# Kernel optimization log

Hardware: AMD Instinct MI355X
Metric: run time of the kernel (lower is better)

The kernel has to match this reference:

```python
import jax, jax.numpy as jnp
import numpy as np

N, E, D, H = 8192, 8, 2048, 2048


def setup_inputs() -> dict:
    key = jax.random.key(0)
    k1, k2, k3, k4 = jax.random.split(key, 4)
    x = jax.random.normal(k1, (N, D), dtype=jnp.float32)
    indices = jax.random.randint(k2, (N, 1), 0, E)  # top_k=1 expert assignment
    W = jax.random.normal(k3, (E, D, H), dtype=jnp.float32) * 0.02
    b = jax.random.normal(k4, (E, H), dtype=jnp.float32) * 0.02
    return {"x": x, "indices": indices, "W": W, "b": b}


def reference(x, indices, W, b):
    # Each token is routed to exactly one expert (top_k=1):
    # expert_id[n] = indices[n, 0]. The torch module loops experts e=0..E-1,
    # gathers tokens with (indices == e).any(-1) (ascending order via nonzero),
    # applies expert e's Linear + ReLU, and concatenates outputs in expert order.
    expert_id = indices[:, 0]                              # [N]
    # Dense dispatch: compute every expert's linear on every token, then pick
    # each token's own expert row (jit-friendly; no data-dependent shapes).
    y_all = jnp.einsum('nd,edh->neh', x, W) + b[None, :, :]  # [N, E, H]
    y = jnp.take_along_axis(y_all, expert_id[:, None, None], axis=1)[:, 1 - 1, :]  # [N, H]
    y = jax.nn.relu(y)
    # Concat in expert order == stable sort of tokens by expert id
    # (nonzero returns ascending indices, so within-expert order is preserved).
    order = jnp.argsort(expert_id)  # stable by default
    return y[order]
```

## Files before the change

### kernel.cpp

```cpp
#include <hip/hip_runtime.h>

#define N_TOK 8192
#define N_EXP 8
#define DIM   2048
#define HID   2048

typedef __attribute__((ext_vector_type(8))) short short8;
typedef __attribute__((ext_vector_type(4))) float f32x4;
typedef __attribute__((ext_vector_type(4))) unsigned short ushort4v;

__device__ inline unsigned short f2bf(float f) {
  unsigned int u = __builtin_bit_cast(unsigned int, f);
  unsigned int r = u + 0x7FFFu + ((u >> 16) & 1u);
  return (unsigned short)(r >> 16);
}

__global__ __launch_bounds__(256) void sort_experts(const int* __restrict__ idx,
                                                    int* __restrict__ perm,
                                                    int* __restrict__ offs) {
  __shared__ int cnt[256][8];
  __shared__ int base[8];
  const int t = threadIdx.x;
  int local[8] = {0,0,0,0,0,0,0,0};
  const int r0 = t * 32;
  for (int i = 0; i < 32; ++i) {
    int e = idx[r0 + i] & 7;
    ++local[e];
  }
#pragma unroll
  for (int e = 0; e < 8; ++e) cnt[t][e] = local[e];
  __syncthreads();
  if (t < 8) {
    int s = 0;
    for (int i = 0; i < 256; ++i) { int v = cnt[i][t]; cnt[i][t] = s; s += v; }
    base[t] = s;
  }
  __syncthreads();
  if (t == 0) {
    int s = 0;
    for (int e = 0; e < 8; ++e) { int v = base[e]; offs[e] = s; base[e] = s; s += v; }
    offs[8] = s;
  }
  __syncthreads();
  int pos[8];
#pragma unroll
  for (int e = 0; e < 8; ++e) pos[e] = base[e] + cnt[t][e];
  for (int i = 0; i < 32; ++i) {
    int r = r0 + i;
    int e = idx[r] & 7;
    perm[pos[e]++] = r;
  }
}

__global__ __launch_bounds__(256) void gather_convert_x(const float* __restrict__ x,
                                                        const int* __restrict__ perm,
                                                        unsigned short* __restrict__ xs) {
  int gid = blockIdx.x * 256 + threadIdx.x;
  int p = gid >> 8;
  int c = gid & 255;
  int src = perm[p];
  const float* sp = x + (size_t)src * DIM + c * 8;
  float4 a = *(const float4*)sp;
  float4 b = *(const float4*)(sp + 4);
  short8 o;
  o[0] = (short)f2bf(a.x); o[1] = (short)f2bf(a.y);
  o[2] = (short)f2bf(a.z); o[3] = (short)f2bf(a.w);
  o[4] = (short)f2bf(b.x); o[5] = (short)f2bf(b.y);
  o[6] = (short)f2bf(b.z); o[7] = (short)f2bf(b.w);
  *(short8*)(xs + (size_t)p * DIM + c * 8) = o;
}

__global__ __launch_bounds__(256) void transpose_convert_w(const float* __restrict__ W,
                                                           unsigned short* __restrict__ Wt) {
  __shared__ unsigned short tile[64][68];
  const int e = blockIdx.z;
  const int d0 = blockIdx.y * 64;
  const int h0 = blockIdx.x * 64;
  const int t = threadIdx.x;
  const int cr = t & 15;
  const int rr = t >> 4;
  const float* Wp = W + ((size_t)e * DIM + d0) * HID + h0;
#pragma unroll
  for (int i = 0; i < 4; ++i) {
    int d = rr + i * 16;
    float4 v = *(const float4*)(Wp + (size_t)d * HID + cr * 4);
    ushort4v o;
    o[0] = f2bf(v.x); o[1] = f2bf(v.y); o[2] = f2bf(v.z); o[3] = f2bf(v.w);
    *(ushort4v*)&tile[d][cr * 4] = o;
  }
  __syncthreads();
  unsigned short* op = Wt + ((size_t)e * HID + h0) * DIM + d0;
#pragma unroll
  for (int i = 0; i < 4; ++i) {
    int h = rr + i * 16;
    ushort4v o;
    o[0] = tile[cr * 4 + 0][h];
    o[1] = tile[cr * 4 + 1][h];
    o[2] = tile[cr * 4 + 2][h];
    o[3] = tile[cr * 4 + 3][h];
    *(ushort4v*)(op + (size_t)h * DIM + cr * 4) = o;
  }
}

#define BM 128
#define BN 128
#define BK 32

__global__ __launch_bounds__(256) void grouped_gemm(const unsigned short* __restrict__ xs,
                                                    const unsigned short* __restrict__ Wt,
                                                    const float* __restrict__ bias,
                                                    const int* __restrict__ offs,
                                                    float* __restrict__ out) {
  const int e   = blockIdx.z;
  const int off = offs[e];
  const int cnt = offs[e + 1] - off;
  const int mt  = blockIdx.y;
  if (mt * BM >= cnt) return;
  const int n0 = blockIdx.x * BN;

  __shared__ __align__(16) unsigned short As[BM * BK];
  __shared__ __align__(16) unsigned short Bs[BN * BK];

  const int t    = threadIdx.x;
  const int wid  = t >> 6;
  const int lane = t & 63;
  const int wr   = wid >> 1, wc = wid & 1;
  const int l15  = lane & 15;
  const int l4   = lane >> 4;

  f32x4 acc[4][4] = {};

  size_t srcA[2], srcB[2];
  const size_t WtE = (size_t)e * DIM * HID;
#pragma unroll
  for (int c = 0; c < 2; ++c) {
    int lin = c * 256 + t;
    int r = lin >> 2, kq = lin & 3;
    int p = off + mt * BM + r;
    if (p > N_TOK - 1) p = N_TOK - 1;
    srcA[c] = (size_t)p * DIM + kq * 8;
    srcB[c] = WtE + (size_t)(n0 + r) * DIM + kq * 8;
  }

  for (int k0 = 0; k0 < DIM; k0 += BK) {
#pragma unroll
    for (int c = 0; c < 2; ++c) {
      __builtin_amdgcn_global_load_lds(
          (const __attribute__((address_space(1))) void*)(xs + srcA[c] + k0),
          (__attribute__((address_space(3))) void*)(As + c * 2048 + t * 8), 16, 0, 0);
      __builtin_amdgcn_global_load_lds(
          (const __attribute__((address_space(1))) void*)(Wt + srcB[c] + k0),
          (__attribute__((address_space(3))) void*)(Bs + c * 2048 + t * 8), 16, 0, 0);
    }
    __syncthreads();

    short8 af[4], bf[4];
#pragma unroll
    for (int m = 0; m < 4; ++m) {
      int row = wr * 64 + m * 16 + l15;
      af[m] = *(const short8*)(As + row * BK + l4 * 8);
    }
#pragma unroll
    for (int n = 0; n < 4; ++n) {
      int row = wc * 64 + n * 16 + l15;
      bf[n] = *(const short8*)(Bs + row * BK + l4 * 8);
    }
#pragma unroll
    for (int m = 0; m < 4; ++m)
#pragma unroll
      for (int n = 0; n < 4; ++n)
        acc[m][n] = __builtin_amdgcn_mfma_f32_16x16x32_bf16(af[m], bf[n], acc[m][n], 0, 0, 0);
    __syncthreads();
  }

#pragma unroll
  for (int n = 0; n < 4; ++n) {
    int col = n0 + wc * 64 + n * 16 + l15;
    float bv = bias[e * HID + col];
#pragma unroll
    for (int m = 0; m < 4; ++m) {
#pragma unroll
      for (int q = 0; q < 4; ++q) {
        int rl = wr * 64 + m * 16 + l4 * 4 + q;
        if (mt * BM + rl < cnt) {
          float v = acc[m][n][q] + bv;
          out[(size_t)(off + mt * BM + rl) * HID + col] = v > 0.f ? v : 0.f;
        }
      }
    }
  }
}

extern "C" void kernel_launch(void* const* d_in, const int* in_sizes, int n_in,
                              void* d_out, int out_size, void* d_ws, size_t ws_size,
                              hipStream_t stream) {
  const float* x   = (const float*)d_in[0];
  const int*   idx = (const int*)d_in[1];
  const float* W   = (const float*)d_in[2];
  const float* b   = (const float*)d_in[3];
  float* out = (float*)d_out;

  char* ws = (char*)d_ws;
  unsigned short* xs = (unsigned short*)ws;
  unsigned short* Wt = (unsigned short*)(ws + (size_t)N_TOK * DIM * 2);
  int* perm = (int*)(ws + (size_t)N_TOK * DIM * 2 + (size_t)N_EXP * DIM * HID * 2);
  int* offs = perm + N_TOK;

  sort_experts<<<1, 256, 0, stream>>>(idx, perm, offs);
  gather_convert_x<<<N_TOK * (DIM / 8) / 256, 256, 0, stream>>>(x, perm, xs);
  transpose_convert_w<<<dim3(HID / 64, DIM / 64, N_EXP), 256, 0, stream>>>(W, Wt);
  grouped_gemm<<<dim3(HID / BN, N_TOK / BM, N_EXP), 256, 0, stream>>>(xs, Wt, b, offs, out);
}
```

Baseline: 188.6 us.

## Persistent job-queue grouped GEMM with swizzled LDS, BK=64 and merged prep kernel

Merges the x gather/convert and W transpose/convert into one prep launch. The sort kernel now also builds a compact list of (expert, m-tile) jobs. The GEMM becomes a persistent kernel of 1024 blocks that pull 128x128 tiles from an atomic queue, so the grid no longer carries empty m-tiles. It uses 2 waves per block with a 64x128 per-wave tile, K-step 64, XOR-swizzled LDS to avoid bank conflicts, and explicit barriers. The cost is fewer waves per block, no double buffering of the loads, and a higher register count from the 4x8 accumulator layout.

Result: slower. 193.9 us (+2.9%).

```diff
diff --git a/kernel.cpp b/kernel.cpp
--- a/kernel.cpp
+++ b/kernel.cpp
@@ -17,7 +17,9 @@
 
 __global__ __launch_bounds__(256) void sort_experts(const int* __restrict__ idx,
                                                     int* __restrict__ perm,
-                                                    int* __restrict__ offs) {
+                                                    int* __restrict__ offs,
+                                                    int* __restrict__ jobs,
+                                                    int* __restrict__ qcnt) {
   __shared__ int cnt[256][8];
   __shared__ int base[8];
   const int t = threadIdx.x;
@@ -37,9 +39,16 @@
   }
   __syncthreads();
   if (t == 0) {
-    int s = 0;
-    for (int e = 0; e < 8; ++e) { int v = base[e]; offs[e] = s; base[e] = s; s += v; }
+    int s = 0, njm = 0;
+    for (int e = 0; e < 8; ++e) {
+      int v = base[e];
+      offs[e] = s; base[e] = s; s += v;
+      int nm = (v + 127) >> 7;
+      for (int mt = 0; mt < nm; ++mt) jobs[1 + njm++] = e | (mt << 8);
+    }
     offs[8] = s;
+    jobs[0] = njm;
+    qcnt[0] = 1024;
   }
   __syncthreads();
   int pos[8];
@@ -52,142 +61,195 @@
   }
 }
 
-__global__ __launch_bounds__(256) void gather_convert_x(const float* __restrict__ x,
-                                                        const int* __restrict__ perm,
-                                                        unsigned short* __restrict__ xs) {
-  int gid = blockIdx.x * 256 + threadIdx.x;
-  int p = gid >> 8;
-  int c = gid & 255;
-  int src = perm[p];
-  const float* sp = x + (size_t)src * DIM + c * 8;
-  float4 a = *(const float4*)sp;
-  float4 b = *(const float4*)(sp + 4);
-  short8 o;
-  o[0] = (short)f2bf(a.x); o[1] = (short)f2bf(a.y);
-  o[2] = (short)f2bf(a.z); o[3] = (short)f2bf(a.w);
-  o[4] = (short)f2bf(b.x); o[5] = (short)f2bf(b.y);
-  o[6] = (short)f2bf(b.z); o[7] = (short)f2bf(b.w);
-  *(short8*)(xs + (size_t)p * DIM + c * 8) = o;
-}
-
-__global__ __launch_bounds__(256) void transpose_convert_w(const float* __restrict__ W,
-                                                           unsigned short* __restrict__ Wt) {
+__global__ __launch_bounds__(256) void prep(const float* __restrict__ x,
+                                            const int* __restrict__ perm,
+                                            unsigned short* __restrict__ xs,
+                                            const float* __restrict__ W,
+                                            unsigned short* __restrict__ Wt) {
   __shared__ unsigned short tile[64][68];
-  const int e = blockIdx.z;
-  const int d0 = blockIdx.y * 64;
-  const int h0 = blockIdx.x * 64;
   const int t = threadIdx.x;
-  const int cr = t & 15;
-  const int rr = t >> 4;
-  const float* Wp = W + ((size_t)e * DIM + d0) * HID + h0;
-#pragma unroll
-  for (int i = 0; i < 4; ++i) {
-    int d = rr + i * 16;
-    float4 v = *(const float4*)(Wp + (size_t)d * HID + cr * 4);
-    ushort4v o;
-    o[0] = f2bf(v.x); o[1] = f2bf(v.y); o[2] = f2bf(v.z); o[3] = f2bf(v.w);
-    *(ushort4v*)&tile[d][cr * 4] = o;
-  }
-  __syncthreads();
-  unsigned short* op = Wt + ((size_t)e * HID + h0) * DIM + d0;
-#pragma unroll
-  for (int i = 0; i < 4; ++i) {
-    int h = rr + i * 16;
-    ushort4v o;
-    o[0] = tile[cr * 4 + 0][h];
-    o[1] = tile[cr * 4 + 1][h];
-    o[2] = tile[cr * 4 + 2][h];
-    o[3] = tile[cr * 4 + 3][h];
-    *(ushort4v*)(op + (size_t)h * DIM + cr * 4) = o;
-  }
-}
-
-#define BM 128
-#define BN 128
-#define BK 32
-
-__global__ __launch_bounds__(256) void grouped_gemm(const unsigned short* __restrict__ xs,
-                                                    const unsigned short* __restrict__ Wt,
-                                                    const float* __restrict__ bias,
-                                                    const int* __restrict__ offs,
-                                                    float* __restrict__ out) {
-  const int e   = blockIdx.z;
-  const int off = offs[e];
-  const int cnt = offs[e + 1] - off;
-  const int mt  = blockIdx.y;
-  if (mt * BM >= cnt) return;
-  const int n0 = blockIdx.x * BN;
-
-  __shared__ __align__(16) unsigned short As[BM * BK];
-  __shared__ __align__(16) unsigned short Bs[BN * BK];
+  if (blockIdx.x < 8192) {
+    int gid = blockIdx.x * 256 + t;
+    int p = gid >> 8;
+    int c = gid & 255;
+    int src = perm[p];
+    const float* sp = x + (size_t)src * DIM + c * 8;
+    float4 a = *(const float4*)sp;
+    float4 b = *(const float4*)(sp + 4);
+    short8 o;
+    o[0] = (short)f2bf(a.x); o[1] = (short)f2bf(a.y);
+    o[2] = (short)f2bf(a.z); o[3] = (short)f2bf(a.w);
+    o[4] = (short)f2bf(b.x); o[5] = (short)f2bf(b.y);
+    o[6] = (short)f2bf(b.z); o[7] = (short)f2bf(b.w);
+    *(short8*)(xs + (size_t)p * DIM + c * 8) = o;
+  } else {
+    const int b = blockIdx.x - 8192;
+    const int e  = b >> 10;
+    const int d0 = ((b >> 5) & 31) * 64;
+    const int h0 = (b & 31) * 64;
+    const int cr = t & 15;
+    const int rr = t >> 4;
+    const float* Wp = W + ((size_t)e * DIM + d0) * HID + h0;
+#pragma unroll
+    for (int i = 0; i < 4; ++i) {
+      int d = rr + i * 16;
+      float4 v = *(const float4*)(Wp + (size_t)d * HID + cr * 4);
+      ushort4v o;
+      o[0] = f2bf(v.x); o[1] = f2bf(v.y); o[2] = f2bf(v.z); o[3] = f2bf(v.w);
+      *(ushort4v*)&tile[d][cr * 4] = o;
+    }
+    __syncthreads();
+    unsigned short* op = Wt + ((size_t)e * HID + h0) * DIM + d0;
+#pragma unroll
+    for (int i = 0; i < 4; ++i) {
+      int h = rr + i * 16;
+      ushort4v o;
+      o[0] = tile[cr * 4 + 0][h];
+      o[1] = tile[cr * 4 + 1][h];
+      o[2] = tile[cr * 4 + 2][h];
+      o[3] = tile[cr * 4 + 3][h];
+      *(ushort4v*)(op + (size_t)h * DIM + cr * 4) = o;
+    }
+  }
+}
+
+#define NKT 32
+
+#define MM(D,A,B) D = __builtin_amdgcn_mfma_f32_16x16x32_bf16(A, B, D, 0, 0, 0)
+#define GLD(SRC, DST) __builtin_amdgcn_global_load_lds( \
+    (const __attribute__((address_space(1))) void*)(SRC), \
+    (__attribute__((address_space(3))) void*)(DST), 16, 0, 0)
+#define BAR() __builtin_amdgcn_s_barrier()
+#define SCHEDB() __builtin_amdgcn_sched_barrier(0)
+
+__global__ __launch_bounds__(128, 2) void grouped_gemm(
+    const unsigned short* __restrict__ xs,
+    const unsigned short* __restrict__ Wt,
+    const float* __restrict__ bias,
+    const int* __restrict__ offs,
+    const int* __restrict__ jobs,
+    int* __restrict__ qcnt,
+    float* __restrict__ out) {
+  __shared__ __align__(16) unsigned short sm[16384];
+  __shared__ int next_j;
 
   const int t    = threadIdx.x;
-  const int wid  = t >> 6;
   const int lane = t & 63;
-  const int wr   = wid >> 1, wc = wid & 1;
+  const int w    = t >> 6;
   const int l15  = lane & 15;
   const int l4   = lane >> 4;
 
-  f32x4 acc[4][4] = {};
-
-  size_t srcA[2], srcB[2];
-  const size_t WtE = (size_t)e * DIM * HID;
-#pragma unroll
-  for (int c = 0; c < 2; ++c) {
-    int lin = c * 256 + t;
-    int r = lin >> 2, kq = lin & 3;
-    int p = off + mt * BM + r;
-    if (p > N_TOK - 1) p = N_TOK - 1;
-    srcA[c] = (size_t)p * DIM + kq * 8;
-    srcB[c] = WtE + (size_t)(n0 + r) * DIM + kq * 8;
-  }
-
-  for (int k0 = 0; k0 < DIM; k0 += BK) {
-#pragma unroll
-    for (int c = 0; c < 2; ++c) {
-      __builtin_amdgcn_global_load_lds(
-          (const __attribute__((address_space(1))) void*)(xs + srcA[c] + k0),
-          (__attribute__((address_space(3))) void*)(As + c * 2048 + t * 8), 16, 0, 0);
-      __builtin_amdgcn_global_load_lds(
-          (const __attribute__((address_space(1))) void*)(Wt + srcB[c] + k0),
-          (__attribute__((address_space(3))) void*)(Bs + c * 2048 + t * 8), 16, 0, 0);
-    }
-    __syncthreads();
-
-    short8 af[4], bf[4];
-#pragma unroll
-    for (int m = 0; m < 4; ++m) {
-      int row = wr * 64 + m * 16 + l15;
-      af[m] = *(const short8*)(As + row * BK + l4 * 8);
-    }
-#pragma unroll
-    for (int n = 0; n < 4; ++n) {
-      int row = wc * 64 + n * 16 + l15;
-      bf[n] = *(const short8*)(Bs + row * BK + l4 * 8);
-    }
+  const int cb0  = (l4 * 8) ^ ((l15 & 7) << 3);
+  const int cb1  = cb0 ^ 32;
+  const int arow = (w * 64 + l15) * 64;
+  const int brow = 8192 + l15 * 64;
+
+  const int r0  = t >> 3;
+  const int keu = ((t & 7) * 8) ^ ((r0 & 7) << 3);
+  const int dA  = t * 8;
+
+  const int total = jobs[0] * 16;
+
+  int j = blockIdx.x;
+  while (j < total) {
+    const int jm  = jobs[1 + (j >> 4)];
+    const int e   = jm & 255;
+    const int mt  = jm >> 8;
+    const int nx  = j & 15;
+    const int off = offs[e];
+    const int cnt = offs[e + 1] - off;
+    const int n0  = nx * 128;
+    const int aBase = off + mt * 128;
+
+    const unsigned int pa = (unsigned)(aBase + r0) * 2048 + keu;
+    const unsigned int pb = ((unsigned)e * 2048 + n0 + r0) * 2048 + keu;
+
+    f32x4 acc[4][8];
 #pragma unroll
     for (int m = 0; m < 4; ++m)
 #pragma unroll
-      for (int n = 0; n < 4; ++n)
-        acc[m][n] = __builtin_amdgcn_mfma_f32_16x16x32_bf16(af[m], bf[n], acc[m][n], 0, 0, 0);
-    __syncthreads();
-  }
-
-#pragma unroll
-  for (int n = 0; n < 4; ++n) {
-    int col = n0 + wc * 64 + n * 16 + l15;
-    float bv = bias[e * HID + col];
-#pragma unroll
-    for (int m = 0; m < 4; ++m) {
-#pragma unroll
-      for (int q = 0; q < 4; ++q) {
-        int rl = wr * 64 + m * 16 + l4 * 4 + q;
-        if (mt * BM + rl < cnt) {
-          float v = acc[m][n][q] + bv;
-          out[(size_t)(off + mt * BM + rl) * HID + col] = v > 0.f ? v : 0.f;
+      for (int n = 0; n < 8; ++n) acc[m][n] = (f32x4){0.f, 0.f, 0.f, 0.f};
+
+#pragma unroll 1
+    for (int T = 0; T < NKT; ++T) {
+      const int k0 = T * 64;
+#pragma unroll
+      for (int ch = 0; ch < 8; ++ch)
+        GLD(xs + pa + ch * 32768 + k0, sm + ch * 1024 + dA);
+#pragma unroll
+      for (int ch = 0; ch < 8; ++ch)
+        GLD(Wt + pb + ch * 32768 + k0, sm + 8192 + ch * 1024 + dA);
+      asm volatile("s_waitcnt vmcnt(0)" ::: "memory");
+      BAR();
+      SCHEDB();
+
+      short8 fa0, fa1, fa2, fa3;
+      short8 fb0, fb1, fb2, fb3, fb4, fb5, fb6, fb7;
+      fa0 = *(const short8*)(sm + arow + 0 * 1024 + cb0);
+      fa1 = *(const short8*)(sm + arow + 1 * 1024 + cb0);
+      fa2 = *(const short8*)(sm + arow + 2 * 1024 + cb0);
+      fa3 = *(const short8*)(sm + arow + 3 * 1024 + cb0);
+      fb0 = *(const short8*)(sm + brow + 0 * 1024 + cb0);
+      fb1 = *(const short8*)(sm + brow + 1 * 1024 + cb0);
+      fb2 = *(const short8*)(sm + brow + 2 * 1024 + cb0);
+      fb3 = *(const short8*)(sm + brow + 3 * 1024 + cb0);
+      fb4 = *(const short8*)(sm + brow + 4 * 1024 + cb0);
+      fb5 = *(const short8*)(sm + brow + 5 * 1024 + cb0);
+      fb6 = *(const short8*)(sm + brow + 6 * 1024 + cb0);
+      fb7 = *(const short8*)(sm + brow + 7 * 1024 + cb0);
+#pragma unroll
+      for (int m = 0; m < 4; ++m) {
+        const short8 fa = (m == 0) ? fa0 : (m == 1) ? fa1 : (m == 2) ? fa2 : fa3;
+        MM(acc[m][0], fa, fb0); MM(acc[m][1], fa, fb1);
+        MM(acc[m][2], fa, fb2); MM(acc[m][3], fa, fb3);
+        MM(acc[m][4], fa, fb4); MM(acc[m][5], fa, fb5);
+        MM(acc[m][6], fa, fb6); MM(acc[m][7], fa, fb7);
+      }
+      fa0 = *(const short8*)(sm + arow + 0 * 1024 + cb1);
+      fa1 = *(const short8*)(sm + arow + 1 * 1024 + cb1);
+      fa2 = *(const short8*)(sm + arow + 2 * 1024 + cb1);
+      fa3 = *(const short8*)(sm + arow + 3 * 1024 + cb1);
+      fb0 = *(const short8*)(sm + brow + 0 * 1024 + cb1);
+      fb1 = *(const short8*)(sm + brow + 1 * 1024 + cb1);
+      fb2 = *(const short8*)(sm + brow + 2 * 1024 + cb1);
+      fb3 = *(const short8*)(sm + brow + 3 * 1024 + cb1);
+      fb4 = *(const short8*)(sm + brow + 4 * 1024 + cb1);
+      fb5 = *(const short8*)(sm + brow + 5 * 1024 + cb1);
+      fb6 = *(const short8*)(sm + brow + 6 * 1024 + cb1);
+      fb7 = *(const short8*)(sm + brow + 7 * 1024 + cb1);
+#pragma unroll
+      for (int m = 0; m < 4; ++m) {
+        const short8 fa = (m == 0) ? fa0 : (m == 1) ? fa1 : (m == 2) ? fa2 : fa3;
+        MM(acc[m][0], fa, fb0); MM(acc[m][1], fa, fb1);
+        MM(acc[m][2], fa, fb2); MM(acc[m][3], fa, fb3);
+        MM(acc[m][4], fa, fb4); MM(acc[m][5], fa, fb5);
+        MM(acc[m][6], fa, fb6); MM(acc[m][7], fa, fb7);
+      }
+      BAR();
+      SCHEDB();
+    }
+
+#pragma unroll
+    for (int n = 0; n < 8; ++n) {
+      int col = n0 + n * 16 + l15;
+      float bv = bias[e * HID + col];
+#pragma unroll
+      for (int m = 0; m < 4; ++m) {
+#pragma unroll
+        for (int q = 0; q < 4; ++q) {
+          int r = w * 64 + m * 16 + l4 * 4 + q;
+          if (mt * 128 + r < cnt) {
+            float v = acc[m][n][q] + bv;
+            out[(size_t)(off + mt * 128 + r) * HID + col] = v > 0.f ? v : 0.f;
+          }
         }
       }
     }
+
+    __syncthreads();
+    if (t == 0) next_j = atomicAdd(qcnt, 1);
+    __syncthreads();
+    j = next_j;
   }
 }
 
@@ -205,9 +267,10 @@
   unsigned short* Wt = (unsigned short*)(ws + (size_t)N_TOK * DIM * 2);
   int* perm = (int*)(ws + (size_t)N_TOK * DIM * 2 + (size_t)N_EXP * DIM * HID * 2);
   int* offs = perm + N_TOK;
-
-  sort_experts<<<1, 256, 0, stream>>>(idx, perm, offs);
-  gather_convert_x<<<N_TOK * (DIM / 8) / 256, 256, 0, stream>>>(x, perm, xs);
-  transpose_convert_w<<<dim3(HID / 64, DIM / 64, N_EXP), 256, 0, stream>>>(W, Wt);
-  grouped_gemm<<<dim3(HID / BN, N_TOK / BM, N_EXP), 256, 0, stream>>>(xs, Wt, b, offs, out);
-}
+  int* jobs = offs + 16;
+  int* qcnt = jobs + 4096;
+
+  sort_experts<<<1, 256, 0, stream>>>(idx, perm, offs, jobs, qcnt);
+  prep<<<16384, 256, 0, stream>>>(x, perm, xs, W, Wt);
+  grouped_gemm<<<1024, 128, 0, stream>>>(xs, Wt, b, offs, jobs, qcnt, out);
+}
```
